# Kernel tuning notes

Hardware: AMD Instinct MI355X
Metric: run time of the kernel (lower is better)

## Reference

```python
import jax, jax.numpy as jnp
import numpy as np

B, S, E = 4, 1024, 512
H = 8
HD = E // H
FF = 4 * E
EPS = 1e-5


def _xavier(key, shape):
    fan_out, fan_in = shape
    std = (2.0 / (fan_in + fan_out)) ** 0.5
    return jax.random.normal(key, shape, dtype=jnp.float32) * std


def setup_inputs() -> dict:
    key = jax.random.key(0)
    ks = jax.random.split(key, 6)
    return {
        "x": jax.random.normal(ks[0], (B, S, E), dtype=jnp.float32),
        "ln1_w": jnp.ones((E,), jnp.float32),
        "ln1_b": jnp.zeros((E,), jnp.float32),
        "qkv_w": _xavier(ks[1], (3 * E, E)),
        "qkv_b": jnp.zeros((3 * E,), jnp.float32),
        "out_w": _xavier(ks[2], (E, E)),
        "out_b": jnp.zeros((E,), jnp.float32),
        "ln2_w": jnp.ones((E,), jnp.float32),
        "ln2_b": jnp.zeros((E,), jnp.float32),
        "fc1_w": _xavier(ks[3], (FF, E)),
        "fc1_b": jnp.zeros((FF,), jnp.float32),
        "fc2_w": _xavier(ks[4], (E, FF)),
        "fc2_b": jnp.zeros((E,), jnp.float32),
    }


def _layernorm(x, w, b):
    mu = jnp.mean(x, -1, keepdims=True)
    var = jnp.mean((x - mu) ** 2, -1, keepdims=True)
    return (x - mu) * jax.lax.rsqrt(var + EPS) * w + b


def _attention(x, qkv_w, qkv_b, out_w, out_b):
    b, s, _ = x.shape
    qkv = x @ qkv_w.T + qkv_b                      # [b, s, 3E]
    q, k, v = jnp.split(qkv, 3, axis=-1)
    def heads(t):
        return t.reshape(b, s, H, HD).transpose(0, 2, 1, 3)  # [b, H, s, hd]
    q, k, v = heads(q), heads(k), heads(v)
    # k is REPLACED by mean of q over seq, broadcast back to full length
    k_mean = jnp.mean(q, axis=2, keepdims=True)    # [b, H, 1, hd]
    k_full = jnp.broadcast_to(k_mean, q.shape)     # [b, H, s, hd]
    scale = HD ** (-0.5)
    attn = jnp.einsum("bhqd,bhkd->bhqk", q, k_full) * scale  # [b, H, s, s]
    attn = jax.nn.softmax(attn, axis=-1)           # rows are constant -> uniform 1/s
    z = jnp.einsum("bhqk,bhkd->bhqd", attn, v)     # [b, H, s, hd]
    z = z.transpose(0, 2, 1, 3).reshape(b, s, H * HD)
    return z @ out_w.T + out_b


def _mlp(x, fc1_w, fc1_b, fc2_w, fc2_b):
    h = jax.nn.gelu(x @ fc1_w.T + fc1_b, approximate=False)
    return h @ fc2_w.T + fc2_b


def reference(x, ln1_w, ln1_b, qkv_w, qkv_b, out_w, out_b,
              ln2_w, ln2_b, fc1_w, fc1_b, fc2_w, fc2_b):
    h = x
    x = _layernorm(x, ln1_w, ln1_b)
    x = _attention(x, qkv_w, qkv_b, out_w, out_b)
    x = x + h
    h = x
    x = _layernorm(x, ln2_w, ln2_b)
    x = _mlp(x, fc1_w, fc1_b, fc2_w, fc2_b)
    return x + h
```

## Files before the change

kernel.cpp:

```cpp
#include <hip/hip_runtime.h>
#include <hip/hip_bf16.h>
#include <math.h>

#define EPSLN 1e-5f

typedef __attribute__((ext_vector_type(8))) short short8;
typedef __attribute__((ext_vector_type(4))) float f32x4;
typedef __attribute__((ext_vector_type(4))) unsigned short u16x4;

__device__ inline unsigned short f2bf(float f){
  unsigned int u = __float_as_uint(f);
  u += 0x7fffu + ((u >> 16) & 1u);
  return (unsigned short)(u >> 16);
}

__device__ inline float wredb(float v){
  #pragma unroll
  for(int o = 1; o < 64; o <<= 1) v += __shfl_xor(v, o, 64);
  return v;
}

__device__ inline float wred(float v){
  #pragma unroll
  for(int o = 32; o > 0; o >>= 1) v += __shfl_down(v, o, 64);
  return v;
}

__global__ __launch_bounds__(256) void prep(
    const float* __restrict__ x, const float* __restrict__ ln1w,
    const float* __restrict__ ln1b, const float* __restrict__ fc1w,
    const float* __restrict__ fc2w, float* __restrict__ colsum,
    unsigned short* __restrict__ w1b, unsigned short* __restrict__ w2b)
{
  __shared__ float red[4][512];
  const int tid = threadIdx.x;
  const int blk = blockIdx.x;
  if(blk < 256){
    const int lane = tid & 63, wv = tid >> 6;
    const int b = blk >> 6, local = blk & 63;
    const f32x4* wp = (const f32x4*)ln1w;
    const f32x4* bp = (const f32x4*)ln1b;
    f32x4 w1 = wp[lane * 2], w2 = wp[lane * 2 + 1];
    f32x4 b1 = bp[lane * 2], b2 = bp[lane * 2 + 1];
    f32x4 a1 = (f32x4)(0.f), a2 = (f32x4)(0.f);
    const int r0 = local * 16 + wv * 4;
    for(int i = 0; i < 4; i++){
      const size_t row = (size_t)b * 1024 + r0 + i;
      const f32x4* xr = (const f32x4*)(x + row * 512);
      f32x4 v1 = xr[lane * 2], v2 = xr[lane * 2 + 1];
      float s = v1[0]+v1[1]+v1[2]+v1[3] + v2[0]+v2[1]+v2[2]+v2[3];
      float q = v1[0]*v1[0]+v1[1]*v1[1]+v1[2]*v1[2]+v1[3]*v1[3]
              + v2[0]*v2[0]+v2[1]*v2[1]+v2[2]*v2[2]+v2[3]*v2[3];
      s = wredb(s); q = wredb(q);
      float mu = s * (1.f / 512.f);
      float rs = rsqrtf(q * (1.f / 512.f) - mu * mu + EPSLN);
      #pragma unroll
      for(int j = 0; j < 4; j++){
        a1[j] += (v1[j] - mu) * rs * w1[j] + b1[j];
        a2[j] += (v2[j] - mu) * rs * w2[j] + b2[j];
      }
    }
    #pragma unroll
    for(int j = 0; j < 4; j++){
      red[wv][lane * 8 + j]     = a1[j];
      red[wv][lane * 8 + 4 + j] = a2[j];
    }
    __syncthreads();
    #pragma unroll
    for(int c = tid; c < 512; c += 256){
      float s = red[0][c] + red[1][c] + red[2][c] + red[3][c];
      atomicAdd(colsum + b * 512 + c, s);
    }
  } else {
    const int w = blk - 256;
    const float* src = (w < 1024) ? fc1w : fc2w;
    unsigned short* dst = (w < 1024) ? w1b : w2b;
    const int off = ((w & 1023) << 10) + tid * 4;
    f32x4 v = *(const f32x4*)(src + off);
    u16x4 r;
    #pragma unroll
    for(int j = 0; j < 4; j++) r[j] = f2bf(v[j]);
    *(u16x4*)(dst + off) = r;
  }
}

__global__ __launch_bounds__(256) void matvec512(
    const float* __restrict__ vec, const float* __restrict__ Wm,
    const float* __restrict__ bias, float* __restrict__ outv, float scale)
{
  int gw = blockIdx.x * 4 + (threadIdx.x >> 6);
  int lane = threadIdx.x & 63;
  int b = gw >> 9, n = gw & 511;
  const f32x4* vr = (const f32x4*)(vec + ((size_t)b << 9));
  const f32x4* wr = (const f32x4*)(Wm + ((size_t)n << 9));
  f32x4 v1 = vr[lane * 2], v2 = vr[lane * 2 + 1];
  f32x4 w1 = wr[lane * 2], w2 = wr[lane * 2 + 1];
  float s = 0.f;
  #pragma unroll
  for(int i = 0; i < 4; i++) s += v1[i] * w1[i] + v2[i] * w2[i];
  s = wred(s);
  if(lane == 0) outv[gw] = s * scale + bias[n];
}

__global__ __launch_bounds__(256) void add_ln2(
    const float* __restrict__ x, const float* __restrict__ arow,
    const float* __restrict__ w, const float* __restrict__ bb,
    unsigned short* __restrict__ xl2)
{
  const int tid = threadIdx.x, lane = tid & 63, wv = tid >> 6;
  const size_t row = (size_t)blockIdx.x * 4 + wv;
  const int b = (int)(row >> 10);
  const f32x4* xr = (const f32x4*)(x + row * 512);
  const f32x4* ar = (const f32x4*)(arow + ((size_t)b << 9));
  f32x4 v1 = xr[lane * 2], v2 = xr[lane * 2 + 1];
  f32x4 r1 = ar[lane * 2], r2 = ar[lane * 2 + 1];
  #pragma unroll
  for(int j = 0; j < 4; j++){ v1[j] += r1[j]; v2[j] += r2[j]; }
  float s = v1[0]+v1[1]+v1[2]+v1[3] + v2[0]+v2[1]+v2[2]+v2[3];
  float q = v1[0]*v1[0]+v1[1]*v1[1]+v1[2]*v1[2]+v1[3]*v1[3]
          + v2[0]*v2[0]+v2[1]*v2[1]+v2[2]*v2[2]+v2[3]*v2[3];
  s = wredb(s); q = wredb(q);
  float mu = s * (1.f / 512.f);
  float rs = rsqrtf(q * (1.f / 512.f) - mu * mu + EPSLN);
  const f32x4* wp = (const f32x4*)w;
  const f32x4* bp = (const f32x4*)bb;
  f32x4 w1 = wp[lane * 2], w2 = wp[lane * 2 + 1];
  f32x4 b1 = bp[lane * 2], b2 = bp[lane * 2 + 1];
  u16x4 o1, o2;
  #pragma unroll
  for(int j = 0; j < 4; j++){
    o1[j] = f2bf((v1[j] - mu) * rs * w1[j] + b1[j]);
    o2[j] = f2bf((v2[j] - mu) * rs * w2[j] + b2[j]);
  }
  u16x4* op = (u16x4*)(xl2 + row * 512 + lane * 8);
  op[0] = o1; op[1] = o2;
}

__device__ inline void gld_lds16(const void* g, void* l){
  __builtin_amdgcn_global_load_lds(
      (const __attribute__((address_space(1))) void*)g,
      (__attribute__((address_space(3))) void*)l, 16, 0, 0);
}

template<int BM, int BN, int EPI>
__global__ __launch_bounds__(256, 2) void gemm_bt(
    const unsigned short* __restrict__ A, const unsigned short* __restrict__ W,
    const float* __restrict__ bias, const float* __restrict__ resx,
    const float* __restrict__ resrow, void* __restrict__ outp,
    int M, int N, int K)
{
  constexpr int BK = 64;
  constexpr int MI = BM / 32, NI = BN / 32;
  constexpr int RPA = BM / 64, RPB = BN / 64;
  __shared__ __align__(16) unsigned short sA[2][BM * BK];
  __shared__ __align__(16) unsigned short sB[2][BN * BK];
  const int tid = threadIdx.x, lane = tid & 63, wv = tid >> 6;
  const int wm = wv >> 1, wn = wv & 1;
  const int m0 = blockIdx.x * BM, n0 = blockIdx.y * BN;

  f32x4 acc[MI][NI];
  #pragma unroll
  for(int i = 0; i < MI; i++)
    #pragma unroll
    for(int j = 0; j < NI; j++) acc[i][j] = (f32x4)(0.f);

  const int rowS = tid >> 2;
  const int colb = (tid & 3) * 16;

  auto stage = [&](int buf, int k0){
    #pragma unroll
    for(int p = 0; p < BM / 32; p++){
      const int h = p / RPA, rb = (p % RPA) * 64;
      const char* g = (const char*)(A + (size_t)(m0 + rb + rowS) * K + k0 + h * 32) + colb;
      gld_lds16(g, (char*)sA[buf] + p * 4096 + tid * 16);
    }
    #pragma unroll
    for(int p = 0; p < BN / 32; p++){
      const int h = p / RPB, rb = (p % RPB) * 64;
      const char* g = (const char*)(W + (size_t)(n0 + rb + rowS) * K + k0 + h * 32) + colb;
      gld_lds16(g, (char*)sB[buf] + p * 4096 + tid * 16);
    }
  };

  const int NT = K / BK;
  stage(0, 0);
  __syncthreads();
  int cur = 0;
  for(int t = 0; t < NT; ++t){
    if(t + 1 < NT) stage(cur ^ 1, (t + 1) * BK);
    short8 af[MI][2], bfr[NI][2];
    const int kof = (lane >> 4) * 8;
    #pragma unroll
    for(int mi = 0; mi < MI; mi++)
      #pragma unroll
      for(int ks = 0; ks < 2; ks++)
        af[mi][ks] = *(const short8*)(sA[cur] + ks * (BM * 32)
                       + (wm * (BM / 2) + mi * 16 + (lane & 15)) * 32 + kof);
    #pragma unroll
    for(int ni = 0; ni < NI; ni++)
      #pragma unroll
      for(int ks = 0; ks < 2; ks++)
        bfr[ni][ks] = *(const short8*)(sB[cur] + ks * (BN * 32)
                       + (wn * (BN / 2) + ni * 16 + (lane & 15)) * 32 + kof);
    #pragma unroll
    for(int mi = 0; mi < MI; mi++)
      #pragma unroll
      for(int ni = 0; ni < NI; ni++){
        acc[mi][ni] = __builtin_amdgcn_mfma_f32_16x16x32_bf16(af[mi][0], bfr[ni][0], acc[mi][ni], 0, 0, 0);
        acc[mi][ni] = __builtin_amdgcn_mfma_f32_16x16x32_bf16(af[mi][1], bfr[ni][1], acc[mi][ni], 0, 0, 0);
      }
    __syncthreads();
    cur ^= 1;
  }

  const int r0 = m0 + wm * (BM / 2) + (lane >> 4) * 4;
  const int c0 = n0 + wn * (BN / 2) + (lane & 15);
  #pragma unroll
  for(int mi = 0; mi < MI; mi++)
    #pragma unroll
    for(int ni = 0; ni < NI; ni++){
      int cc = c0 + ni * 16;
      float bi = bias[cc];
      #pragma unroll
      for(int j = 0; j < 4; j++){
        int rr = r0 + mi * 16 + j;
        float v = acc[mi][ni][j] + bi;
        if constexpr(EPI == 0){
          float u = v + 0.044715f * v * v * v;
          float gl = v / (1.f + __expf(-1.5957691216f * u));
          ((unsigned short*)outp)[(size_t)rr * N + cc] = f2bf(gl);
        } else {
          v += resx[(size_t)rr * N + cc] + resrow[((rr >> 10) << 9) + cc];
          ((float*)outp)[(size_t)rr * N + cc] = v;
        }
      }
    }
}

extern "C" void kernel_launch(void* const* d_in, const int* in_sizes, int n_in,
                              void* d_out, int out_size, void* d_ws, size_t ws_size,
                              hipStream_t stream)
{
  (void)in_sizes; (void)n_in; (void)out_size; (void)ws_size;
  const float* x    = (const float*)d_in[0];
  const float* ln1w = (const float*)d_in[1];
  const float* ln1b = (const float*)d_in[2];
  const float* qkvw = (const float*)d_in[3];
  const float* qkvb = (const float*)d_in[4];
  const float* outw = (const float*)d_in[5];
  const float* outb = (const float*)d_in[6];
  const float* ln2w = (const float*)d_in[7];
  const float* ln2b = (const float*)d_in[8];
  const float* fc1w = (const float*)d_in[9];
  const float* fc1b = (const float*)d_in[10];
  const float* fc2w = (const float*)d_in[11];
  const float* fc2b = (const float*)d_in[12];

  char* ws = (char*)d_ws;
  float*          colsum = (float*)ws;
  float*          vmean  = (float*)(ws + 8192);
  float*          arow   = (float*)(ws + 16384);
  unsigned short* xl2    = (unsigned short*)(ws + (1u << 20));
  unsigned short* w1b    = (unsigned short*)(ws + (5u << 20));
  unsigned short* w2b    = (unsigned short*)(ws + (7u << 20));
  unsigned short* hact   = (unsigned short*)(ws + (9u << 20));

  hipMemsetAsync(colsum, 0, 2048 * 4, stream);
  prep<<<2304, 256, 0, stream>>>(x, ln1w, ln1b, fc1w, fc2w, colsum, w1b, w2b);
  matvec512<<<512, 256, 0, stream>>>(colsum, qkvw + 2 * 512 * 512, qkvb + 1024, vmean, 1.f / 1024.f);
  matvec512<<<512, 256, 0, stream>>>(vmean, outw, outb, arow, 1.f);
  add_ln2<<<1024, 256, 0, stream>>>(x, arow, ln2w, ln2b, xl2);
  gemm_bt<128, 128, 0><<<dim3(32, 16), 256, 0, stream>>>(
      xl2, w1b, fc1b, nullptr, nullptr, hact, 4096, 2048, 512);
  gemm_bt<64, 64, 1><<<dim3(64, 8), 256, 0, stream>>>(
      hact, w2b, fc2b, x, arow, d_out, 4096, 512, 2048);
}
```

Baseline: 66.34 us.

## Replace atomic colsum with per-block partials and deepen BK for fc2 GEMM

```diff
diff --git a/kernel.cpp b/kernel.cpp
--- a/kernel.cpp
+++ b/kernel.cpp
@@ -29,7 +29,7 @@
 __global__ __launch_bounds__(256) void prep(
     const float* __restrict__ x, const float* __restrict__ ln1w,
     const float* __restrict__ ln1b, const float* __restrict__ fc1w,
-    const float* __restrict__ fc2w, float* __restrict__ colsum,
+    const float* __restrict__ fc2w, float* __restrict__ part,
     unsigned short* __restrict__ w1b, unsigned short* __restrict__ w2b)
 {
   __shared__ float red[4][512];
@@ -67,10 +67,8 @@
     }
     __syncthreads();
     #pragma unroll
-    for(int c = tid; c < 512; c += 256){
-      float s = red[0][c] + red[1][c] + red[2][c] + red[3][c];
-      atomicAdd(colsum + b * 512 + c, s);
-    }
+    for(int c = tid; c < 512; c += 256)
+      part[(size_t)blk * 512 + c] = red[0][c] + red[1][c] + red[2][c] + red[3][c];
   } else {
     const int w = blk - 256;
     const float* src = (w < 1024) ? fc1w : fc2w;
@@ -84,9 +82,41 @@
   }
 }
 
+__global__ __launch_bounds__(256) void colsum_matvec(
+    const float* __restrict__ part, const float* __restrict__ qkvw,
+    const float* __restrict__ qkvb, float* __restrict__ vmean)
+{
+  __shared__ float cs[512];
+  const int tid = threadIdx.x, lane = tid & 63, wv = tid >> 6;
+  const int b = blockIdx.x >> 5;
+  const int nb = (blockIdx.x & 31) * 16;
+  #pragma unroll
+  for(int c = tid; c < 512; c += 256){
+    float s = 0.f;
+    const float* pp = part + (size_t)(b * 64) * 512 + c;
+    #pragma unroll 8
+    for(int p = 0; p < 64; p++) s += pp[(size_t)p * 512];
+    cs[c] = s;
+  }
+  __syncthreads();
+  const f32x4* c4 = (const f32x4*)cs;
+  f32x4 v1 = c4[lane * 2], v2 = c4[lane * 2 + 1];
+  #pragma unroll
+  for(int o = 0; o < 4; o++){
+    int n = nb + wv * 4 + o;
+    const f32x4* wr = (const f32x4*)(qkvw + (size_t)(1024 + n) * 512);
+    f32x4 w1 = wr[lane * 2], w2 = wr[lane * 2 + 1];
+    float s = 0.f;
+    #pragma unroll
+    for(int i = 0; i < 4; i++) s += v1[i] * w1[i] + v2[i] * w2[i];
+    s = wred(s);
+    if(lane == 0) vmean[b * 512 + n] = s * (1.f / 1024.f) + qkvb[1024 + n];
+  }
+}
+
 __global__ __launch_bounds__(256) void matvec512(
     const float* __restrict__ vec, const float* __restrict__ Wm,
-    const float* __restrict__ bias, float* __restrict__ outv, float scale)
+    const float* __restrict__ bias, float* __restrict__ outv)
 {
   int gw = blockIdx.x * 4 + (threadIdx.x >> 6);
   int lane = threadIdx.x & 63;
@@ -99,7 +129,7 @@
   #pragma unroll
   for(int i = 0; i < 4; i++) s += v1[i] * w1[i] + v2[i] * w2[i];
   s = wred(s);
-  if(lane == 0) outv[gw] = s * scale + bias[n];
+  if(lane == 0) outv[gw] = s + bias[n];
 }
 
 __global__ __launch_bounds__(256) void add_ln2(
@@ -142,15 +172,17 @@
       (__attribute__((address_space(3))) void*)l, 16, 0, 0);
 }
 
-template<int BM, int BN, int EPI>
+template<int BM, int BN, int BK, int EPI>
 __global__ __launch_bounds__(256, 2) void gemm_bt(
     const unsigned short* __restrict__ A, const unsigned short* __restrict__ W,
     const float* __restrict__ bias, const float* __restrict__ resx,
     const float* __restrict__ resrow, void* __restrict__ outp,
     int M, int N, int K)
 {
-  constexpr int BK = 64;
   constexpr int MI = BM / 32, NI = BN / 32;
+  constexpr int KS = BK / 32;
+  constexpr int PA = BM * BK / 2048;
+  constexpr int PB = BN * BK / 2048;
   constexpr int RPA = BM / 64, RPB = BN / 64;
   __shared__ __align__(16) unsigned short sA[2][BM * BK];
   __shared__ __align__(16) unsigned short sB[2][BN * BK];
@@ -169,13 +201,13 @@
 
   auto stage = [&](int buf, int k0){
     #pragma unroll
-    for(int p = 0; p < BM / 32; p++){
+    for(int p = 0; p < PA; p++){
       const int h = p / RPA, rb = (p % RPA) * 64;
       const char* g = (const char*)(A + (size_t)(m0 + rb + rowS) * K + k0 + h * 32) + colb;
       gld_lds16(g, (char*)sA[buf] + p * 4096 + tid * 16);
     }
     #pragma unroll
-    for(int p = 0; p < BN / 32; p++){
+    for(int p = 0; p < PB; p++){
       const int h = p / RPB, rb = (p % RPB) * 64;
       const char* g = (const char*)(W + (size_t)(n0 + rb + rowS) * K + k0 + h * 32) + colb;
       gld_lds16(g, (char*)sB[buf] + p * 4096 + tid * 16);
@@ -188,27 +220,27 @@
   int cur = 0;
   for(int t = 0; t < NT; ++t){
     if(t + 1 < NT) stage(cur ^ 1, (t + 1) * BK);
-    short8 af[MI][2], bfr[NI][2];
+    short8 af[MI][KS], bfr[NI][KS];
     const int kof = (lane >> 4) * 8;
     #pragma unroll
     for(int mi = 0; mi < MI; mi++)
       #pragma unroll
-      for(int ks = 0; ks < 2; ks++)
+      for(int ks = 0; ks < KS; ks++)
         af[mi][ks] = *(const short8*)(sA[cur] + ks * (BM * 32)
                        + (wm * (BM / 2) + mi * 16 + (lane & 15)) * 32 + kof);
     #pragma unroll
     for(int ni = 0; ni < NI; ni++)
       #pragma unroll
-      for(int ks = 0; ks < 2; ks++)
+      for(int ks = 0; ks < KS; ks++)
         bfr[ni][ks] = *(const short8*)(sB[cur] + ks * (BN * 32)
                        + (wn * (BN / 2) + ni * 16 + (lane & 15)) * 32 + kof);
     #pragma unroll
     for(int mi = 0; mi < MI; mi++)
       #pragma unroll
-      for(int ni = 0; ni < NI; ni++){
-        acc[mi][ni] = __builtin_amdgcn_mfma_f32_16x16x32_bf16(af[mi][0], bfr[ni][0], acc[mi][ni], 0, 0, 0);
-        acc[mi][ni] = __builtin_amdgcn_mfma_f32_16x16x32_bf16(af[mi][1], bfr[ni][1], acc[mi][ni], 0, 0, 0);
-      }
+      for(int ni = 0; ni < NI; ni++)
+        #pragma unroll
+        for(int ks = 0; ks < KS; ks++)
+          acc[mi][ni] = __builtin_amdgcn_mfma_f32_16x16x32_bf16(af[mi][ks], bfr[ni][ks], acc[mi][ni], 0, 0, 0);
     __syncthreads();
     cur ^= 1;
   }
@@ -257,21 +289,20 @@
   const float* fc2b = (const float*)d_in[12];
 
   char* ws = (char*)d_ws;
-  float*          colsum = (float*)ws;
-  float*          vmean  = (float*)(ws + 8192);
-  float*          arow   = (float*)(ws + 16384);
+  float*          part   = (float*)ws;
+  float*          vmean  = (float*)(ws + (1u << 19));
+  float*          arow   = (float*)(ws + (1u << 19) + 8192);
   unsigned short* xl2    = (unsigned short*)(ws + (1u << 20));
   unsigned short* w1b    = (unsigned short*)(ws + (5u << 20));
   unsigned short* w2b    = (unsigned short*)(ws + (7u << 20));
   unsigned short* hact   = (unsigned short*)(ws + (9u << 20));
 
-  hipMemsetAsync(colsum, 0, 2048 * 4, stream);
-  prep<<<2304, 256, 0, stream>>>(x, ln1w, ln1b, fc1w, fc2w, colsum, w1b, w2b);
-  matvec512<<<512, 256, 0, stream>>>(colsum, qkvw + 2 * 512 * 512, qkvb + 1024, vmean, 1.f / 1024.f);
-  matvec512<<<512, 256, 0, stream>>>(vmean, outw, outb, arow, 1.f);
+  prep<<<2304, 256, 0, stream>>>(x, ln1w, ln1b, fc1w, fc2w, part, w1b, w2b);
+  colsum_matvec<<<128, 256, 0, stream>>>(part, qkvw, qkvb, vmean);
+  matvec512<<<512, 256, 0, stream>>>(vmean, outw, outb, arow);
   add_ln2<<<1024, 256, 0, stream>>>(x, arow, ln2w, ln2b, xl2);
-  gemm_bt<128, 128, 0><<<dim3(32, 16), 256, 0, stream>>>(
+  gemm_bt<128, 128, 64, 0><<<dim3(32, 16), 256, 0, stream>>>(
       xl2, w1b, fc1b, nullptr, nullptr, hact, 4096, 2048, 512);
-  gemm_bt<64, 64, 1><<<dim3(64, 8), 256, 0, stream>>>(
+  gemm_bt<64, 64, 128, 1><<<dim3(64, 8), 256, 0, stream>>>(
       hact, w2b, fc2b, x, arow, d_out, 4096, 512, 2048);
 }
```

After: 63.04 us, median of 3. 1.05x faster.
